# Optimization experiments

Hardware: AMD Instinct MI355X
Metric: run time of the kernel (lower is better)

The kernel has to match this reference:

```python
import jax, jax.numpy as jnp
import numpy as np

T, H = 4096, 2048

def _glorot(key, shape):
    return jax.random.uniform(key, shape, minval=-1.0, maxval=1.0) * jnp.sqrt(2.0 / sum(shape))

def setup_inputs() -> dict:
    key = jax.random.key(0)
    kx, ka, kb = jax.random.split(key, 3)
    x = jax.random.normal(kx, (T, H), dtype=jnp.float32)
    a_mat = _glorot(ka, (H,)).astype(jnp.float32)          # |a| < 1 -> stable recurrence
    b_mat = _glorot(kb, (H, H)).astype(jnp.float32)
    return {"x": x, "a_mat": a_mat, "b_mat": b_mat}

def reference(x, a_mat, b_mat):
    # s_t = b_mat.T @ x_t for all t, done as one GEMM: (T,H) @ (H,H)
    s = x @ b_mat  # (T, H)
    def step(h, s_t):
        h = jnp.tanh(a_mat * h + s_t)
        return h, h
    h0 = jnp.zeros_like(a_mat)
    _, h_seq = jax.lax.scan(step, h0, s)
    return h_seq  # (T, H)
```

## Files before the change

kernel.cpp:

```cpp
#include <hip/hip_runtime.h>
#include <stdint.h>
#include <stddef.h>

#define Tdim 4096
#define Hdim 2048

typedef short short8 __attribute__((ext_vector_type(8)));
typedef float floatx4 __attribute__((ext_vector_type(4)));

__device__ __forceinline__ unsigned short f2bf(float f) {
  uint32_t u = __float_as_uint(f);
  u += 0x7fffu + ((u >> 16) & 1u);
  return (unsigned short)(u >> 16);
}

__device__ __forceinline__ void load_lds16(const void* g, void* l) {
  __builtin_amdgcn_global_load_lds(
      (__attribute__((address_space(1))) unsigned int*)(uintptr_t)g,
      (__attribute__((address_space(3))) unsigned int*)l,
      16, 0, 0);
}

__device__ __forceinline__ float tanh_fast(float z) {
  float e = __expf(z + z);
  return 1.0f - __fdividef(2.0f, e + 1.0f);
}

__device__ __forceinline__ short8 lds_read8(const unsigned short* p) {
  return *(const short8*)__builtin_assume_aligned(p, 16);
}

#define SYNC_DRAIN()                                                   \
  do {                                                                 \
    asm volatile("s_waitcnt vmcnt(0) lgkmcnt(0)" ::: "memory");        \
    __syncthreads();                                                   \
  } while (0)

__global__ __launch_bounds__(256) void cvt_kernel(const float* __restrict__ x,
                                                  const float* __restrict__ b,
                                                  unsigned short* __restrict__ xbf,
                                                  unsigned short* __restrict__ bt) {
  __shared__ unsigned short tile[64 * 65];
  const int t = threadIdx.x;
  if (blockIdx.x < 4096) {
    size_t i = ((size_t)blockIdx.x * 256 + t) * 8;
    float4 f0 = *(const float4*)(x + i);
    float4 f1 = *(const float4*)(x + i + 4);
    union { unsigned short u[8]; uint4 v; } o;
    o.u[0] = f2bf(f0.x); o.u[1] = f2bf(f0.y); o.u[2] = f2bf(f0.z); o.u[3] = f2bf(f0.w);
    o.u[4] = f2bf(f1.x); o.u[5] = f2bf(f1.y); o.u[6] = f2bf(f1.z); o.u[7] = f2bf(f1.w);
    *(uint4*)(xbf + i) = o.v;
    return;
  }
  const int tb = blockIdx.x - 4096;
  const int bj = tb & 31;
  const int bi = tb >> 5;
  {
    const int r0 = t >> 4, c4 = (t & 15) * 4;
#pragma unroll
    for (int p = 0; p < 4; ++p) {
      int r = r0 + p * 16;
      float4 v = *(const float4*)(b + (size_t)(bi * 64 + r) * Hdim + bj * 64 + c4);
      tile[r * 65 + c4 + 0] = f2bf(v.x);
      tile[r * 65 + c4 + 1] = f2bf(v.y);
      tile[r * 65 + c4 + 2] = f2bf(v.z);
      tile[r * 65 + c4 + 3] = f2bf(v.w);
    }
  }
  __syncthreads();
  {
    const int n = t >> 2, kq = (t & 3) * 16;
    union { unsigned short u[16]; uint4 v[2]; } o;
#pragma unroll
    for (int q = 0; q < 16; ++q) o.u[q] = tile[(kq + q) * 65 + n];
    uint4* dst = (uint4*)(bt + (size_t)(bj * 64 + n) * Hdim + bi * 64 + kq);
    dst[0] = o.v[0];
    dst[1] = o.v[1];
  }
}

__global__ __launch_bounds__(512, 4) void gemm_scan_kernel(const unsigned short* __restrict__ A,
                                                           const unsigned short* __restrict__ Bt,
                                                           const float* __restrict__ a_mat,
                                                           float* __restrict__ out) {
  __shared__ alignas(16) union SM {
    struct {
      unsigned short sA[2][128 * 64];
      unsigned short sB[2][128 * 64];
      unsigned short sAw[2][8 * 64];
    } st;
    float s_tile[136 * 129];
  } sm;

  const int tid = threadIdx.x;
  const int bm = blockIdx.x, bn = blockIdx.y;
  const int wave = tid >> 6, lane = tid & 63;
  const int wm = (wave >> 2) * 64;
  const int wn = (wave & 3) * 32;
  const int l15 = lane & 15, quad = lane >> 4;
  const int l7 = l15 & 7;

  const int swz = ((tid & 7) ^ ((tid >> 3) & 7)) * 8;
  const unsigned short* aSrc = A + ((size_t)(bm * 128 + (tid >> 3)) * Hdim + swz);
  const unsigned short* bSrc = Bt + ((size_t)(bn * 128 + (tid >> 3)) * Hdim + swz);
  const int tw0 = (bm > 0) ? bm * 128 - 8 : 0;
  const int wswz = ((lane & 7) ^ ((lane >> 3) & 7)) * 8;
  const unsigned short* wSrc = A + ((size_t)(tw0 + (lane >> 3)) * Hdim + wswz);

  floatx4 acc[4][2] = {};
  floatx4 accw[2] = {};

  auto stage = [&](int buf, int k0) {
    unsigned short* aDst = &sm.st.sA[buf][tid * 8];
    unsigned short* bDst = &sm.st.sB[buf][tid * 8];
#pragma unroll
    for (int c = 0; c < 2; ++c) {
      load_lds16(aSrc + (size_t)c * 64 * Hdim + k0, aDst + c * 4096);
      load_lds16(bSrc + (size_t)c * 64 * Hdim + k0, bDst + c * 4096);
    }
    if (wave == 7) load_lds16(wSrc + k0, &sm.st.sAw[buf][lane * 8]);
  };

  auto compute = [&](int buf) {
#pragma unroll
    for (int kk = 0; kk < 64; kk += 32) {
      const int coff = (((kk >> 3) + quad) ^ l7) * 8;
      short8 av[4], bv[2];
#pragma unroll
      for (int i = 0; i < 4; ++i)
        av[i] = lds_read8(&sm.st.sA[buf][(wm + i * 16 + l15) * 64 + coff]);
#pragma unroll
      for (int j = 0; j < 2; ++j)
        bv[j] = lds_read8(&sm.st.sB[buf][(wn + j * 16 + l15) * 64 + coff]);
#pragma unroll
      for (int i = 0; i < 4; ++i)
#pragma unroll
        for (int j = 0; j < 2; ++j)
          acc[i][j] = __builtin_amdgcn_mfma_f32_16x16x32_bf16(av[i], bv[j], acc[i][j], 0, 0, 0);
      if (wm == 0) {
        short8 aw = lds_read8(&sm.st.sAw[buf][l7 * 64 + coff]);
#pragma unroll
        for (int j = 0; j < 2; ++j)
          accw[j] = __builtin_amdgcn_mfma_f32_16x16x32_bf16(aw, bv[j], accw[j], 0, 0, 0);
      }
    }
  };

  stage(0, 0);
  SYNC_DRAIN();
  for (int it = 0; it < 32; it += 2) {
    stage(1, (it + 1) * 64);
    compute(0);
    SYNC_DRAIN();
    if (it + 2 < 32) stage(0, (it + 2) * 64);
    compute(1);
    SYNC_DRAIN();
  }

  if (wm == 0 && quad < 2) {
#pragma unroll
    for (int j = 0; j < 2; ++j)
#pragma unroll
      for (int r = 0; r < 4; ++r)
        sm.s_tile[(quad * 4 + r) * 129 + wn + j * 16 + l15] = accw[j][r];
  }
#pragma unroll
  for (int i = 0; i < 4; ++i)
#pragma unroll
    for (int j = 0; j < 2; ++j)
#pragma unroll
      for (int r = 0; r < 4; ++r)
        sm.s_tile[(8 + wm + i * 16 + quad * 4 + r) * 129 + wn + j * 16 + l15] = acc[i][j][r];
  SYNC_DRAIN();

  const int col = tid & 127;
  const int chunk = tid >> 7;
  const float aj = a_mat[bn * 128 + col];
  float h = 0.0f;
  const int row0 = 8 + chunk * 32;
  if (!(bm == 0 && chunk == 0)) {
#pragma unroll
    for (int r = row0 - 8; r < row0; ++r)
      h = tanh_fast(fmaf(aj, h, sm.s_tile[r * 129 + col]));
  }
  const size_t gbase = (size_t)(bm * 128 + chunk * 32) * Hdim + bn * 128 + col;
#pragma unroll 4
  for (int r2 = 0; r2 < 32; ++r2) {
    h = tanh_fast(fmaf(aj, h, sm.s_tile[(row0 + r2) * 129 + col]));
    out[gbase + (size_t)r2 * Hdim] = h;
  }
}

extern "C" void kernel_launch(void* const* d_in, const int* in_sizes, int n_in,
                              void* d_out, int out_size, void* d_ws, size_t ws_size,
                              hipStream_t stream) {
  const float* x = (const float*)d_in[0];
  const float* a = (const float*)d_in[1];
  const float* b = (const float*)d_in[2];
  float* out = (float*)d_out;

  unsigned short* ws = (unsigned short*)d_ws;
  unsigned short* xbf = ws;
  unsigned short* btb = xbf + (size_t)Tdim * Hdim;

  hipLaunchKernelGGL(cvt_kernel, dim3(4096 + (Hdim / 64) * (Hdim / 64)), dim3(256), 0, stream,
                     x, b, xbf, btb);
  hipLaunchKernelGGL(gemm_scan_kernel, dim3(Tdim / 128, Hdim / 128), dim3(512), 0, stream,
                     xbf, btb, a, out);
}
```

Before: 139.7 us.

## Fuse x fp32-to-bf16 conversion into GEMM A-tile staging via registers

The separate pass that converts x to bf16 in workspace is removed. The GEMM kernel now reads fp32 x directly through register loads, converts it to bf16, and writes it into LDS after each compute step, with the load issued before compute to overlap latency. This drops one full write and re-read of the bf16 copy of x. In exchange, each tile reads twice the A bytes (fp32), the GEMM holds more registers, and conversion ALU work lands inside the main loop. Each of the 16 column blocks re-reads x, so the extra fp32 traffic is multiplied.

```diff
diff --git a/kernel.cpp b/kernel.cpp
--- a/kernel.cpp
+++ b/kernel.cpp
@@ -7,6 +7,7 @@
 
 typedef short short8 __attribute__((ext_vector_type(8)));
 typedef float floatx4 __attribute__((ext_vector_type(4)));
+typedef float f32x4 __attribute__((ext_vector_type(4)));
 
 __device__ __forceinline__ unsigned short f2bf(float f) {
   uint32_t u = __float_as_uint(f);
@@ -30,29 +31,22 @@
   return *(const short8*)__builtin_assume_aligned(p, 16);
 }
 
+typedef __attribute__((address_space(1))) const f32x4* gptrf4;
+__device__ __forceinline__ f32x4 glb_readf4(const float* p) {
+  return *(gptrf4)(uintptr_t)__builtin_assume_aligned(p, 16);
+}
+
 #define SYNC_DRAIN()                                                   \
   do {                                                                 \
     asm volatile("s_waitcnt vmcnt(0) lgkmcnt(0)" ::: "memory");        \
     __syncthreads();                                                   \
   } while (0)
 
-__global__ __launch_bounds__(256) void cvt_kernel(const float* __restrict__ x,
-                                                  const float* __restrict__ b,
-                                                  unsigned short* __restrict__ xbf,
+__global__ __launch_bounds__(256) void cvt_kernel(const float* __restrict__ b,
                                                   unsigned short* __restrict__ bt) {
   __shared__ unsigned short tile[64 * 65];
   const int t = threadIdx.x;
-  if (blockIdx.x < 4096) {
-    size_t i = ((size_t)blockIdx.x * 256 + t) * 8;
-    float4 f0 = *(const float4*)(x + i);
-    float4 f1 = *(const float4*)(x + i + 4);
-    union { unsigned short u[8]; uint4 v; } o;
-    o.u[0] = f2bf(f0.x); o.u[1] = f2bf(f0.y); o.u[2] = f2bf(f0.z); o.u[3] = f2bf(f0.w);
-    o.u[4] = f2bf(f1.x); o.u[5] = f2bf(f1.y); o.u[6] = f2bf(f1.z); o.u[7] = f2bf(f1.w);
-    *(uint4*)(xbf + i) = o.v;
-    return;
-  }
-  const int tb = blockIdx.x - 4096;
+  const int tb = blockIdx.x;
   const int bj = tb & 31;
   const int bi = tb >> 5;
   {
@@ -79,7 +73,7 @@
   }
 }
 
-__global__ __launch_bounds__(512, 4) void gemm_scan_kernel(const unsigned short* __restrict__ A,
+__global__ __launch_bounds__(512, 4) void gemm_scan_kernel(const float* __restrict__ X,
                                                            const unsigned short* __restrict__ Bt,
                                                            const float* __restrict__ a_mat,
                                                            float* __restrict__ out) {
@@ -101,24 +95,56 @@
   const int l7 = l15 & 7;
 
   const int swz = ((tid & 7) ^ ((tid >> 3) & 7)) * 8;
-  const unsigned short* aSrc = A + ((size_t)(bm * 128 + (tid >> 3)) * Hdim + swz);
+  const float* aSrc = X + ((size_t)(bm * 128 + (tid >> 3)) * Hdim + swz);
   const unsigned short* bSrc = Bt + ((size_t)(bn * 128 + (tid >> 3)) * Hdim + swz);
   const int tw0 = (bm > 0) ? bm * 128 - 8 : 0;
   const int wswz = ((lane & 7) ^ ((lane >> 3) & 7)) * 8;
-  const unsigned short* wSrc = A + ((size_t)(tw0 + (lane >> 3)) * Hdim + wswz);
+  const float* wSrc = X + ((size_t)(tw0 + (lane >> 3)) * Hdim + wswz);
 
   floatx4 acc[4][2] = {};
   floatx4 accw[2] = {};
 
-  auto stage = [&](int buf, int k0) {
+  auto stageB = [&](int buf, int k0) {
+    unsigned short* bDst = &sm.st.sB[buf][tid * 8];
+#pragma unroll
+    for (int c = 0; c < 2; ++c)
+      load_lds16(bSrc + (size_t)c * 64 * Hdim + k0, bDst + c * 4096);
+  };
+
+  struct AReg { f32x4 f[4]; f32x4 w[2]; };
+  auto loadA = [&](AReg& r, int k0) {
+#pragma unroll
+    for (int c = 0; c < 2; ++c) {
+      r.f[c * 2 + 0] = glb_readf4(aSrc + (size_t)c * 64 * Hdim + k0);
+      r.f[c * 2 + 1] = glb_readf4(aSrc + (size_t)c * 64 * Hdim + k0 + 4);
+    }
+    if (wave == 7) {
+      r.w[0] = glb_readf4(wSrc + k0);
+      r.w[1] = glb_readf4(wSrc + k0 + 4);
+    }
+  };
+
+  auto writeA = [&](int buf, const AReg& r) {
     unsigned short* aDst = &sm.st.sA[buf][tid * 8];
-    unsigned short* bDst = &sm.st.sB[buf][tid * 8];
 #pragma unroll
     for (int c = 0; c < 2; ++c) {
-      load_lds16(aSrc + (size_t)c * 64 * Hdim + k0, aDst + c * 4096);
-      load_lds16(bSrc + (size_t)c * 64 * Hdim + k0, bDst + c * 4096);
-    }
-    if (wave == 7) load_lds16(wSrc + k0, &sm.st.sAw[buf][lane * 8]);
+      union { unsigned short u[8]; short8 v; } o;
+#pragma unroll
+      for (int q = 0; q < 4; ++q) {
+        o.u[q] = f2bf(r.f[c * 2 + 0][q]);
+        o.u[4 + q] = f2bf(r.f[c * 2 + 1][q]);
+      }
+      *(short8*)__builtin_assume_aligned(aDst + c * 4096, 16) = o.v;
+    }
+    if (wave == 7) {
+      union { unsigned short u[8]; short8 v; } o;
+#pragma unroll
+      for (int q = 0; q < 4; ++q) {
+        o.u[q] = f2bf(r.w[0][q]);
+        o.u[4 + q] = f2bf(r.w[1][q]);
+      }
+      *(short8*)__builtin_assume_aligned(&sm.st.sAw[buf][lane * 8], 16) = o.v;
+    }
   };
 
   auto compute = [&](int buf) {
@@ -146,14 +172,24 @@
     }
   };
 
-  stage(0, 0);
+  AReg ar;
+
+  loadA(ar, 0);
+  stageB(0, 0);
+  writeA(0, ar);
   SYNC_DRAIN();
   for (int it = 0; it < 32; it += 2) {
-    stage(1, (it + 1) * 64);
+    loadA(ar, (it + 1) * 64);
+    stageB(1, (it + 1) * 64);
     compute(0);
+    writeA(1, ar);
     SYNC_DRAIN();
-    if (it + 2 < 32) stage(0, (it + 2) * 64);
+    if (it + 2 < 32) {
+      loadA(ar, (it + 2) * 64);
+      stageB(0, (it + 2) * 64);
+    }
     compute(1);
+    if (it + 2 < 32) writeA(0, ar);
     SYNC_DRAIN();
   }
 
@@ -199,12 +235,10 @@
   const float* b = (const float*)d_in[2];
   float* out = (float*)d_out;
 
-  unsigned short* ws = (unsigned short*)d_ws;
-  unsigned short* xbf = ws;
-  unsigned short* btb = xbf + (size_t)Tdim * Hdim;
-
-  hipLaunchKernelGGL(cvt_kernel, dim3(4096 + (Hdim / 64) * (Hdim / 64)), dim3(256), 0, stream,
-                     x, b, xbf, btb);
+  unsigned short* btb = (unsigned short*)d_ws;
+
+  hipLaunchKernelGGL(cvt_kernel, dim3((Hdim / 64) * (Hdim / 64)), dim3(256), 0, stream,
+                     b, btb);
   hipLaunchKernelGGL(gemm_scan_kernel, dim3(Tdim / 128, Hdim / 128), dim3(512), 0, stream,
-                     xbf, btb, a, out);
-}
+                     x, btb, a, out);
+}
```

Result: slower. 148.0 us (+6.0%).
